# Optimization experiments

Measured on AMD Instinct MI355X. Metric: run time of the kernel, lower is better.

Reference implementation:

```python
import jax, jax.numpy as jnp
import numpy as np

N_NODES = 25000
N_EDGES = 400000
IN = 128
HID = [64, 64, 128]
HEADS = [4, 4, 1]
SLOPE = 0.01  # F.leaky_relu default


def _xavier(key, shape):
    fan_out, fan_in = shape
    std = (2.0 / (fan_in + fan_out)) ** 0.5
    return std * jax.random.normal(key, shape, dtype=jnp.float32)


def setup_inputs() -> dict:
    key = jax.random.key(0)
    ks = jax.random.split(key, 24)
    inp = {}
    inp['x'] = jax.random.normal(ks[0], (N_NODES, IN), dtype=jnp.float32)
    inp['edge_weight'] = jax.random.uniform(ks[1], (N_EDGES,), dtype=jnp.float32)
    inp['edge_src'] = jax.random.randint(ks[2], (N_EDGES,), 0, N_NODES)
    inp['edge_dst'] = jax.random.randint(ks[3], (N_EDGES,), 0, N_NODES)
    inp['pos_src'] = jax.random.randint(ks[4], (100000,), 0, N_NODES)
    inp['pos_dst'] = jax.random.randint(ks[5], (100000,), 0, N_NODES)
    inp['neg_src'] = jax.random.randint(ks[6], (100000,), 0, N_NODES)
    inp['neg_dst'] = jax.random.randint(ks[7], (100000,), 0, N_NODES)
    # GAT layer params: fc weight [H*F, in], attn vector [F], bias [H*F]
    dims_in = [IN, HID[0] * HEADS[0], HID[1] * HEADS[1]]
    for l in range(3):
        H, F = HEADS[l], HID[l]
        inp[f'W{l}'] = _xavier(ks[8 + 2 * l], (H * F, dims_in[l]))
        inp[f'a{l}'] = _xavier(ks[9 + 2 * l], (1, F)).reshape(F)
        inp[f'b{l}'] = jnp.zeros((H * F,), dtype=jnp.float32)
    # predictor MLP: 128 -> 64 -> 32 -> 1 (Linear with bias)
    d = HID[2]
    inp['pW1'] = _xavier(ks[14], (d // 2, d)); inp['pb1'] = jnp.zeros((d // 2,), jnp.float32)
    inp['pW2'] = _xavier(ks[15], (d // 4, d // 2)); inp['pb2'] = jnp.zeros((d // 4,), jnp.float32)
    inp['pW3'] = _xavier(ks[16], (1, d // 4)); inp['pb3'] = jnp.zeros((1,), jnp.float32)
    return inp


def _leaky(x, slope=SLOPE):
    return jnp.where(x >= 0, x, slope * x)


def _gat_layer(x, W, a, b, src, dst, ew, H, F):
    N = x.shape[0]
    h = (x @ W.T).reshape(N, H, F)               # [N,H,F]
    hs = h[src]                                   # [E,H,F] gathered src feats
    # GATv2-style score: attn_fc(q_src + k_dst) per head
    score = jnp.einsum('ehf,f->eh', hs + h[dst], a)   # [E,H]
    e = _leaky(score + jnp.log1p(ew)[:, None])         # [E,H]
    # segment softmax over edges grouped by destination node
    m = jax.ops.segment_max(e, dst, num_segments=N)    # [N,H]
    m = jnp.where(jnp.isfinite(m), m, 0.0)             # guard empty segments
    ex = jnp.exp(e - m[dst])
    s = jax.ops.segment_sum(ex, dst, num_segments=N)   # [N,H]
    alpha = ex / jnp.maximum(s[dst], 1e-20)            # [E,H]
    out = jax.ops.segment_sum(alpha[:, :, None] * hs, dst, num_segments=N)  # [N,H,F]
    return out.reshape(N, H * F) + b


def _predictor(z, pW1, pb1, pW2, pb2, pW3, pb3):
    z = _leaky(z @ pW1.T + pb1, 0.2)
    z = _leaky(z @ pW2.T + pb2, 0.2)
    return z @ pW3.T + pb3


def reference(x, edge_weight, W0, a0, b0, W1, a1, b1, W2, a2, b2,
              pW1, pb1, pW2, pb2, pW3, pb3,
              edge_src, edge_dst, pos_src, pos_dst, neg_src, neg_dst):
    h = _gat_layer(x, W0, a0, b0, edge_src, edge_dst, edge_weight, HEADS[0], HID[0])
    h = _leaky(h)
    h = _gat_layer(h, W1, a1, b1, edge_src, edge_dst, edge_weight, HEADS[1], HID[1])
    h = _leaky(h)
    h = _gat_layer(h, W2, a2, b2, edge_src, edge_dst, edge_weight, HEADS[2], HID[2])
    gat_embedding = h
    h_pos = _predictor(h[pos_src] * h[pos_dst], pW1, pb1, pW2, pb2, pW3, pb3)
    h_neg = _predictor(h[neg_src] * h[neg_dst], pW1, pb1, pW2, pb2, pW3, pb3)
    return (h_pos, h_neg, gat_embedding)
```

## Files before the change

kernel.cpp:

```cpp
#include <hip/hip_runtime.h>
#include <math.h>

#define N_IN 128

__device__ __forceinline__ float leaky01(float x) { return x >= 0.f ? x : 0.01f * x; }
__device__ __forceinline__ float leaky02(float x) { return x >= 0.f ? x : 0.2f * x; }

__global__ void k_count(const int* __restrict__ edst, int* __restrict__ deg, int E) {
    int e = blockIdx.x * 256 + threadIdx.x;
    if (e < E) atomicAdd(&deg[edst[e]], 1);
}

__global__ void k_scan1(const int* __restrict__ deg, int* __restrict__ rowptr,
                        int* __restrict__ bsum, int n) {
    __shared__ int s[256];
    int b = blockIdx.x, t = threadIdx.x;
    int idx = b * 256 + t;
    int v = (idx < n) ? deg[idx] : 0;
    s[t] = v;
    __syncthreads();
    for (int off = 1; off < 256; off <<= 1) {
        int x = (t >= off) ? s[t - off] : 0;
        __syncthreads();
        s[t] += x;
        __syncthreads();
    }
    if (idx < n) rowptr[idx + 1] = s[t];
    if (t == 255) bsum[b] = s[255];
}

__global__ void k_scan2(const int* __restrict__ bsum, int* __restrict__ boff, int nb) {
    __shared__ int s[128];
    int t = threadIdx.x;
    int v = (t < nb) ? bsum[t] : 0;
    s[t] = v;
    __syncthreads();
    for (int off = 1; off < 128; off <<= 1) {
        int x = (t >= off) ? s[t - off] : 0;
        __syncthreads();
        s[t] += x;
        __syncthreads();
    }
    if (t < nb) boff[t] = s[t] - v;
}

__global__ void k_scan3(int* __restrict__ rowptr, const int* __restrict__ boff, int n) {
    int idx = blockIdx.x * 256 + threadIdx.x;
    if (idx < n) rowptr[idx + 1] += boff[idx >> 8];
    if (idx == 0) rowptr[0] = 0;
}

__global__ void k_fill(const int* __restrict__ esrc, const int* __restrict__ edst,
                       const float* __restrict__ ew, const int* __restrict__ rowptr,
                       int* __restrict__ cursor, int* __restrict__ eid,
                       int* __restrict__ csrc, float* __restrict__ clew, int E) {
    int e = blockIdx.x * 256 + threadIdx.x;
    if (e >= E) return;
    int d = edst[e];
    int slot = rowptr[d] + atomicAdd(&cursor[d], 1);
    eid[slot] = e;
    csrc[slot] = esrc[e];
    clew[slot] = log1pf(ew[e]);
}

__global__ void k_sortseg(const int* __restrict__ rowptr, int* __restrict__ eid,
                          int* __restrict__ csrc, float* __restrict__ clew, int n) {
    int v = blockIdx.x * 256 + threadIdx.x;
    if (v >= n) return;
    int b = rowptr[v], e = rowptr[v + 1];
    for (int i = b + 1; i < e; i++) {
        int ke = eid[i], ks = csrc[i];
        float kl = clew[i];
        int j = i - 1;
        while (j >= b && eid[j] > ke) {
            eid[j + 1] = eid[j]; csrc[j + 1] = csrc[j]; clew[j + 1] = clew[j];
            j--;
        }
        eid[j + 1] = ke; csrc[j + 1] = ks; clew[j + 1] = kl;
    }
}

__global__ __launch_bounds__(256) void k_gemm(const float* __restrict__ X,
                                              const float* __restrict__ W,
                                              float* __restrict__ C,
                                              int N, int K, int M,
                                              const float* __restrict__ avec,
                                              float* __restrict__ qaOut,
                                              int H, int F) {
    __shared__ float Xs[16][68];
    __shared__ float Ws[16][132];
    __shared__ float qred[64][17];
    int r0 = blockIdx.y * 64;
    int c0 = blockIdx.x * 128;
    int t = threadIdx.x;
    int ty = t >> 4, tx = t & 15;

    float acc[4][8];
#pragma unroll
    for (int i = 0; i < 4; i++)
#pragma unroll
        for (int j = 0; j < 8; j++) acc[i][j] = 0.f;

    int lr = t >> 2;
    int lk = (t & 3) * 4;
    bool xok = (r0 + lr) < N;
    const float* Xp = X + (size_t)(r0 + lr) * K + lk;
    int wr = t >> 1;
    int wk = (t & 1) * 8;
    const float* Wp = W + (size_t)(c0 + wr) * K + wk;

    for (int k0 = 0; k0 < K; k0 += 16) {
        float4 xv = xok ? *(const float4*)(Xp + k0) : make_float4(0.f, 0.f, 0.f, 0.f);
        float4 wv0 = *(const float4*)(Wp + k0);
        float4 wv1 = *(const float4*)(Wp + k0 + 4);
        __syncthreads();
        Xs[lk + 0][lr] = xv.x; Xs[lk + 1][lr] = xv.y;
        Xs[lk + 2][lr] = xv.z; Xs[lk + 3][lr] = xv.w;
        Ws[wk + 0][wr] = wv0.x; Ws[wk + 1][wr] = wv0.y;
        Ws[wk + 2][wr] = wv0.z; Ws[wk + 3][wr] = wv0.w;
        Ws[wk + 4][wr] = wv1.x; Ws[wk + 5][wr] = wv1.y;
        Ws[wk + 6][wr] = wv1.z; Ws[wk + 7][wr] = wv1.w;
        __syncthreads();
#pragma unroll
        for (int k = 0; k < 16; k++) {
            float4 a = *(const float4*)&Xs[k][ty * 4];
            float4 b0 = *(const float4*)&Ws[k][tx * 8];
            float4 b1 = *(const float4*)&Ws[k][tx * 8 + 4];
            float av[4] = {a.x, a.y, a.z, a.w};
            float bv[8] = {b0.x, b0.y, b0.z, b0.w, b1.x, b1.y, b1.z, b1.w};
#pragma unroll
            for (int i = 0; i < 4; i++)
#pragma unroll
                for (int j = 0; j < 8; j++) acc[i][j] += av[i] * bv[j];
        }
    }

#pragma unroll
    for (int i = 0; i < 4; i++) {
        int row = r0 + ty * 4 + i;
        if (row < N) {
            float4 v0 = make_float4(acc[i][0], acc[i][1], acc[i][2], acc[i][3]);
            float4 v1 = make_float4(acc[i][4], acc[i][5], acc[i][6], acc[i][7]);
            *(float4*)&C[(size_t)row * M + c0 + tx * 8] = v0;
            *(float4*)&C[(size_t)row * M + c0 + tx * 8 + 4] = v1;
        }
    }

    if (qaOut) {
        int f0 = (c0 + tx * 8) & (F - 1);
        float4 a0 = *(const float4*)&avec[f0];
        float4 a1 = *(const float4*)&avec[f0 + 4];
#pragma unroll
        for (int i = 0; i < 4; i++) {
            float s = acc[i][0] * a0.x + acc[i][1] * a0.y + acc[i][2] * a0.z + acc[i][3] * a0.w
                    + acc[i][4] * a1.x + acc[i][5] * a1.y + acc[i][6] * a1.z + acc[i][7] * a1.w;
            qred[ty * 4 + i][tx] = s;
        }
        __syncthreads();
        if (t < 64) {
            int R = r0 + t;
            if (R < N) {
                float s0 = 0.f, s1 = 0.f;
#pragma unroll
                for (int x = 0; x < 8; x++) { s0 += qred[t][x]; s1 += qred[t][x + 8]; }
                if (F == 64) {
                    int hb = c0 >> 6;
                    qaOut[(size_t)R * H + hb] = s0;
                    qaOut[(size_t)R * H + hb + 1] = s1;
                } else {
                    qaOut[R] = s0 + s1;
                }
            }
        }
    }
}

template <int H, int F, int VW, bool LOUT>
__global__ __launch_bounds__(256) void k_fagg(const float* __restrict__ feat,
                                              const float* __restrict__ qa,
                                              const float* __restrict__ bias,
                                              const int* __restrict__ rowptr,
                                              const int* __restrict__ csr_src,
                                              const float* __restrict__ csr_lew,
                                              float* __restrict__ out, int N) {
    constexpr int M = H * F;
    constexpr int CACHE = 128;
    constexpr int EPP = 64 / H;
    __shared__ int sh_src[4][CACHE];
    __shared__ float sh_sc[4][CACHE * H];
    int w = threadIdx.x >> 6, l = threadIdx.x & 63;
    int n = blockIdx.x * 4 + w;
    if (n >= N) return;
    int beg = rowptr[n];
    int deg = rowptr[n + 1] - beg;
    int c = l * VW;
    const int hh = c / F;

    float acc0[VW], acc1[VW];
#pragma unroll
    for (int j = 0; j < VW; j++) { acc0[j] = 0.f; acc1[j] = 0.f; }

    if (deg > 0) {
        if (deg <= CACHE) {
            const int e0 = l / H;
            const int h = l & (H - 1);
            float qd = qa[(size_t)n * H + h];
            float mx = -1e30f;
            for (int i0 = 0; i0 < deg; i0 += EPP) {
                int e = i0 + e0;
                if (e < deg) {
                    int src = csr_src[beg + e];
                    float lw = csr_lew[beg + e];
                    if (h == 0) sh_src[w][e] = src;
                    float sc = leaky01(qa[(size_t)src * H + h] + qd + lw);
                    sh_sc[w][e * H + h] = sc;
                    mx = fmaxf(mx, sc);
                }
            }
            for (int off = 32; off >= H; off >>= 1)
                mx = fmaxf(mx, __shfl_xor(mx, off, 64));
            float sm = 0.f;
            for (int i0 = 0; i0 < deg; i0 += EPP) {
                int e = i0 + e0;
                if (e < deg) sm += __expf(sh_sc[w][e * H + h] - mx);
            }
            for (int off = 32; off >= H; off >>= 1)
                sm += __shfl_xor(sm, off, 64);
            float inv = 1.f / fmaxf(sm, 1e-20f);
            for (int i0 = 0; i0 < deg; i0 += EPP) {
                int e = i0 + e0;
                if (e < deg)
                    sh_sc[w][e * H + h] = __expf(sh_sc[w][e * H + h] - mx) * inv;
            }
            int i = 0;
            for (; i + 4 <= deg; i += 4) {
                int s0 = sh_src[w][i], s1 = sh_src[w][i + 1];
                int s2 = sh_src[w][i + 2], s3 = sh_src[w][i + 3];
                float a0 = sh_sc[w][i * H + hh], a1 = sh_sc[w][(i + 1) * H + hh];
                float a2 = sh_sc[w][(i + 2) * H + hh], a3 = sh_sc[w][(i + 3) * H + hh];
                float f0[VW], f1[VW], f2[VW], f3[VW];
                if (VW == 4) {
                    float4 v0 = *(const float4*)&feat[(size_t)s0 * M + c];
                    float4 v1 = *(const float4*)&feat[(size_t)s1 * M + c];
                    float4 v2 = *(const float4*)&feat[(size_t)s2 * M + c];
                    float4 v3 = *(const float4*)&feat[(size_t)s3 * M + c];
                    f0[0] = v0.x; f0[1] = v0.y; f0[2] = v0.z; f0[3] = v0.w;
                    f1[0] = v1.x; f1[1] = v1.y; f1[2] = v1.z; f1[3] = v1.w;
                    f2[0] = v2.x; f2[1] = v2.y; f2[2] = v2.z; f2[3] = v2.w;
                    f3[0] = v3.x; f3[1] = v3.y; f3[2] = v3.z; f3[3] = v3.w;
                } else {
                    float2 v0 = *(const float2*)&feat[(size_t)s0 * M + c];
                    float2 v1 = *(const float2*)&feat[(size_t)s1 * M + c];
                    float2 v2 = *(const float2*)&feat[(size_t)s2 * M + c];
                    float2 v3 = *(const float2*)&feat[(size_t)s3 * M + c];
                    f0[0] = v0.x; f0[1] = v0.y;
                    f1[0] = v1.x; f1[1] = v1.y;
                    f2[0] = v2.x; f2[1] = v2.y;
                    f3[0] = v3.x; f3[1] = v3.y;
                }
#pragma unroll
                for (int j = 0; j < VW; j++) {
                    acc0[j] += a0 * f0[j] + a1 * f1[j];
                    acc1[j] += a2 * f2[j] + a3 * f3[j];
                }
            }
            for (; i < deg; ++i) {
                int s0 = sh_src[w][i];
                float a0 = sh_sc[w][i * H + hh];
                if (VW == 4) {
                    float4 v0 = *(const float4*)&feat[(size_t)s0 * M + c];
                    acc0[0] += a0 * v0.x; acc0[1] += a0 * v0.y;
                    acc0[2] += a0 * v0.z; acc0[3] += a0 * v0.w;
                } else {
                    float2 v0 = *(const float2*)&feat[(size_t)s0 * M + c];
                    acc0[0] += a0 * v0.x; acc0[1] += a0 * v0.y;
                }
            }
        } else {
            float qd[H];
#pragma unroll
            for (int h = 0; h < H; h++) qd[h] = qa[(size_t)n * H + h];
            int end = beg + deg;
            float mx[H];
#pragma unroll
            for (int h = 0; h < H; h++) mx[h] = -1e30f;
            for (int i = beg + l; i < end; i += 64) {
                int src = csr_src[i];
                float lw = csr_lew[i];
#pragma unroll
                for (int h = 0; h < H; h++)
                    mx[h] = fmaxf(mx[h], leaky01(qa[(size_t)src * H + h] + qd[h] + lw));
            }
#pragma unroll
            for (int h = 0; h < H; h++) {
                for (int off = 32; off > 0; off >>= 1)
                    mx[h] = fmaxf(mx[h], __shfl_xor(mx[h], off, 64));
            }
            float sm[H];
#pragma unroll
            for (int h = 0; h < H; h++) sm[h] = 0.f;
            for (int i = beg + l; i < end; i += 64) {
                int src = csr_src[i];
                float lw = csr_lew[i];
#pragma unroll
                for (int h = 0; h < H; h++)
                    sm[h] += __expf(leaky01(qa[(size_t)src * H + h] + qd[h] + lw) - mx[h]);
            }
#pragma unroll
            for (int h = 0; h < H; h++) {
                for (int off = 32; off > 0; off >>= 1)
                    sm[h] += __shfl_xor(sm[h], off, 64);
            }
            float inv[H];
#pragma unroll
            for (int h = 0; h < H; h++) inv[h] = 1.f / fmaxf(sm[h], 1e-20f);

            for (int c0 = 0; c0 < deg; c0 += 64) {
                int cn = min(64, deg - c0);
                if (l < cn) {
                    int src = csr_src[beg + c0 + l];
                    float lw = csr_lew[beg + c0 + l];
                    sh_src[w][l] = src;
#pragma unroll
                    for (int h = 0; h < H; h++)
                        sh_sc[w][l * H + h] =
                            __expf(leaky01(qa[(size_t)src * H + h] + qd[h] + lw) - mx[h]) * inv[h];
                }
                for (int i = 0; i < cn; i++) {
                    int s0 = sh_src[w][i];
                    float a0 = sh_sc[w][i * H + hh];
                    if (VW == 4) {
                        float4 v0 = *(const float4*)&feat[(size_t)s0 * M + c];
                        acc0[0] += a0 * v0.x; acc0[1] += a0 * v0.y;
                        acc0[2] += a0 * v0.z; acc0[3] += a0 * v0.w;
                    } else {
                        float2 v0 = *(const float2*)&feat[(size_t)s0 * M + c];
                        acc0[0] += a0 * v0.x; acc0[1] += a0 * v0.y;
                    }
                }
            }
        }
    }

#pragma unroll
    for (int j = 0; j < VW; j++) {
        float r = acc0[j] + acc1[j] + bias[c + j];
        if (LOUT) r = leaky01(r);
        out[(size_t)n * M + c + j] = r;
    }
}

__global__ __launch_bounds__(256) void k_predf6(const float* __restrict__ h2,
                                                const int* __restrict__ ps, const int* __restrict__ pd,
                                                const int* __restrict__ ns, const int* __restrict__ nd,
                                                const float* __restrict__ W1, const float* __restrict__ b1,
                                                const float* __restrict__ W2, const float* __restrict__ b2,
                                                const float* __restrict__ W3, const float* __restrict__ b3,
                                                float* __restrict__ out, int npos, int ntot) {
    __shared__ float Zs[128 * 36];
    __shared__ float Wc[32 * 68];
    __shared__ int sp[128], dp[128];

    int t = threadIdx.x;
    int p0 = blockIdx.x * 128;
    int ty2 = t >> 3;
    int tx2 = t & 7;

    if (t < 128) {
        int pr = p0 + t;
        int s = 0, d = 0;
        if (pr < ntot) {
            if (pr < npos) { s = ps[pr]; d = pd[pr]; }
            else           { s = ns[pr - npos]; d = nd[pr - npos]; }
        }
        sp[t] = s; dp[t] = d;
    }
    __syncthreads();

    float acc[4][8];
#pragma unroll
    for (int i = 0; i < 4; i++)
#pragma unroll
        for (int j = 0; j < 8; j++) acc[i][j] = 0.f;

    int sr = t >> 3;
    int sq = t & 7;

    for (int kc = 0; kc < 128; kc += 32) {
#pragma unroll
        for (int it = 0; it < 4; ++it) {
            int r = it * 32 + sr;
            int s = sp[r], d = dp[r];
            float4 a = *(const float4*)&h2[(size_t)s * 128 + kc + sq * 4];
            float4 b = *(const float4*)&h2[(size_t)d * 128 + kc + sq * 4];
            *(float4*)&Zs[r * 36 + sq * 4] =
                make_float4(a.x * b.x, a.y * b.y, a.z * b.z, a.w * b.w);
        }
        {
            int out_ = t & 63;
            int kh = (t >> 6) * 8;
            const float* wr = W1 + (size_t)out_ * 128 + kc + kh;
#pragma unroll
            for (int c = 0; c < 2; c++) {
                float4 wv = *(const float4*)(wr + c * 4);
                Wc[(kh + c * 4 + 0) * 68 + out_] = wv.x;
                Wc[(kh + c * 4 + 1) * 68 + out_] = wv.y;
                Wc[(kh + c * 4 + 2) * 68 + out_] = wv.z;
                Wc[(kh + c * 4 + 3) * 68 + out_] = wv.w;
            }
        }
        __syncthreads();
#pragma unroll
        for (int k4 = 0; k4 < 8; ++k4) {
            float4 a4[4];
#pragma unroll
            for (int i = 0; i < 4; i++)
                a4[i] = *(const float4*)&Zs[(ty2 + 32 * i) * 36 + k4 * 4];
#pragma unroll
            for (int kk = 0; kk < 4; ++kk) {
                float4 bA = *(const float4*)&Wc[(k4 * 4 + kk) * 68 + tx2 * 8];
                float4 bB = *(const float4*)&Wc[(k4 * 4 + kk) * 68 + tx2 * 8 + 4];
                float bv[8] = {bA.x, bA.y, bA.z, bA.w, bB.x, bB.y, bB.z, bB.w};
#pragma unroll
                for (int i = 0; i < 4; i++) {
                    float a = (kk == 0) ? a4[i].x : (kk == 1) ? a4[i].y : (kk == 2) ? a4[i].z : a4[i].w;
#pragma unroll
                    for (int j = 0; j < 8; j++) acc[i][j] += a * bv[j];
                }
            }
        }
        __syncthreads();
    }

    {
        float4 b1a = *(const float4*)&b1[tx2 * 8];
        float4 b1b = *(const float4*)&b1[tx2 * 8 + 4];
        float bb[8] = {b1a.x, b1a.y, b1a.z, b1a.w, b1b.x, b1b.y, b1b.z, b1b.w};
#pragma unroll
        for (int i = 0; i < 4; i++)
#pragma unroll
            for (int j = 0; j < 8; j++) acc[i][j] += bb[j];
    }

    float t2[32];
#pragma unroll
    for (int o = 0; o < 32; o++) t2[o] = b2[o];

    if (tx2 < 4) {
#pragma unroll
        for (int i = 0; i < 4; i++) {
            int row = ty2 + 32 * i;
            *(float4*)&Zs[row * 36 + tx2 * 8] =
                make_float4(acc[i][0], acc[i][1], acc[i][2], acc[i][3]);
            *(float4*)&Zs[row * 36 + tx2 * 8 + 4] =
                make_float4(acc[i][4], acc[i][5], acc[i][6], acc[i][7]);
        }
    }
    __syncthreads();
    if (t < 128) {
        for (int j = 0; j < 32; j += 4) {
            float4 v4 = *(const float4*)&Zs[t * 36 + j];
            float v0 = leaky02(v4.x), v1 = leaky02(v4.y), v2 = leaky02(v4.z), v3 = leaky02(v4.w);
#pragma unroll
            for (int o = 0; o < 32; o++) {
                const float* w2 = W2 + (size_t)o * 64 + j;
                t2[o] += v0 * w2[0] + v1 * w2[1] + v2 * w2[2] + v3 * w2[3];
            }
        }
    }
    __syncthreads();
    if (tx2 >= 4) {
#pragma unroll
        for (int i = 0; i < 4; i++) {
            int row = ty2 + 32 * i;
            *(float4*)&Zs[row * 36 + (tx2 - 4) * 8] =
                make_float4(acc[i][0], acc[i][1], acc[i][2], acc[i][3]);
            *(float4*)&Zs[row * 36 + (tx2 - 4) * 8 + 4] =
                make_float4(acc[i][4], acc[i][5], acc[i][6], acc[i][7]);
        }
    }
    __syncthreads();
    if (t < 128) {
        for (int j = 0; j < 32; j += 4) {
            float4 v4 = *(const float4*)&Zs[t * 36 + j];
            float v0 = leaky02(v4.x), v1 = leaky02(v4.y), v2 = leaky02(v4.z), v3 = leaky02(v4.w);
#pragma unroll
            for (int o = 0; o < 32; o++) {
                const float* w2 = W2 + (size_t)o * 64 + 32 + j;
                t2[o] += v0 * w2[0] + v1 * w2[1] + v2 * w2[2] + v3 * w2[3];
            }
        }
        float o3 = b3[0];
#pragma unroll
        for (int o = 0; o < 32; o++) o3 += leaky02(t2[o]) * W3[o];
        if (p0 + t < ntot) out[p0 + t] = o3;
    }
}

extern "C" void kernel_launch(void* const* d_in, const int* in_sizes, int n_in,
                              void* d_out, int out_size, void* d_ws, size_t ws_size,
                              hipStream_t stream) {
    const float* x    = (const float*)d_in[0];
    const float* ew   = (const float*)d_in[1];
    const int* esrc   = (const int*)d_in[2];
    const int* edst   = (const int*)d_in[3];
    const int* pos_s  = (const int*)d_in[4];
    const int* pos_d  = (const int*)d_in[5];
    const int* neg_s  = (const int*)d_in[6];
    const int* neg_d  = (const int*)d_in[7];
    const float* W0 = (const float*)d_in[8];
    const float* a0 = (const float*)d_in[9];
    const float* b0 = (const float*)d_in[10];
    const float* W1 = (const float*)d_in[11];
    const float* a1 = (const float*)d_in[12];
    const float* b1 = (const float*)d_in[13];
    const float* W2 = (const float*)d_in[14];
    const float* a2 = (const float*)d_in[15];
    const float* b2 = (const float*)d_in[16];
    const float* pW1 = (const float*)d_in[17];
    const float* pb1 = (const float*)d_in[18];
    const float* pW2 = (const float*)d_in[19];
    const float* pb2 = (const float*)d_in[20];
    const float* pW3 = (const float*)d_in[21];
    const float* pb3 = (const float*)d_in[22];

    const int N = in_sizes[0] / N_IN;
    const int E = in_sizes[1];
    const int NP = in_sizes[4];

    size_t off = 0;
    auto alloc = [&](size_t bytes) {
        void* p = (char*)d_ws + off;
        off += (bytes + 255) & ~(size_t)255;
        return p;
    };
    int* deg      = (int*)alloc((size_t)N * 4);
    int* cursor   = (int*)alloc((size_t)N * 4);
    int* rowptr   = (int*)alloc((size_t)(N + 1) * 4);
    int* bsum     = (int*)alloc(512);
    int* boff     = (int*)alloc(512);
    int* csr_eid  = (int*)alloc((size_t)E * 4);
    int* csr_src  = (int*)alloc((size_t)E * 4);
    float* csr_lew = (float*)alloc((size_t)E * 4);
    float* qa     = (float*)alloc((size_t)N * 4 * 4);
    float* A      = (float*)alloc((size_t)N * 256 * 4);
    float* B      = (float*)alloc((size_t)N * 256 * 4);
    (void)ws_size; (void)n_in; (void)out_size;

    float* out_pred = (float*)d_out;
    float* emb      = (float*)d_out + 2 * NP;

    hipMemsetAsync(deg, 0, (size_t)N * 4, stream);
    hipMemsetAsync(cursor, 0, (size_t)N * 4, stream);

    int eb = (E + 255) / 256;
    int nb = (N + 255) / 256;
    k_count<<<eb, 256, 0, stream>>>(edst, deg, E);
    k_scan1<<<nb, 256, 0, stream>>>(deg, rowptr, bsum, N);
    k_scan2<<<1, 128, 0, stream>>>(bsum, boff, nb);
    k_scan3<<<nb, 256, 0, stream>>>(rowptr, boff, N);
    k_fill<<<eb, 256, 0, stream>>>(esrc, edst, ew, rowptr, cursor, csr_eid, csr_src, csr_lew, E);
    k_sortseg<<<(N + 255) / 256, 256, 0, stream>>>(rowptr, csr_eid, csr_src, csr_lew, N);

    int rb = (N + 63) / 64;
    int sb = (N + 3) / 4;

    k_gemm<<<dim3(2, rb), 256, 0, stream>>>(x, W0, A, N, 128, 256, a0, qa, 4, 64);
    k_fagg<4, 64, 4, true><<<sb, 256, 0, stream>>>(A, qa, b0, rowptr, csr_src, csr_lew, B, N);

    k_gemm<<<dim3(2, rb), 256, 0, stream>>>(B, W1, A, N, 256, 256, a1, qa, 4, 64);
    k_fagg<4, 64, 4, true><<<sb, 256, 0, stream>>>(A, qa, b1, rowptr, csr_src, csr_lew, B, N);

    k_gemm<<<dim3(1, rb), 256, 0, stream>>>(B, W2, A, N, 256, 128, a2, qa, 1, 128);
    k_fagg<1, 128, 2, false><<<sb, 256, 0, stream>>>(A, qa, b2, rowptr, csr_src, csr_lew, emb, N);

    int ntot = 2 * NP;
    k_predf6<<<(ntot + 127) / 128, 256, 0, stream>>>(emb, pos_s, pos_d, neg_s, neg_d,
                                                     pW1, pb1, pW2, pb2, pW3, pb3,
                                                     out_pred, NP, ntot);
}
```

Before: 487.8 us.

## Pack CSR into int4 records, warp-parallel segment sort, smaller predictor tiles

Edge id, source and log1p weight are packed into one int4 CSR record, so k_fill does one store per edge and the aggregation kernels do one 16-byte load instead of separate arrays. The per-node serial insertion sort runs one thread per node; it is replaced by a wavefront-per-node rank sort using shuffles for degree up to 64, with a single-lane fallback for larger segments. The predictor kernel tile shrinks from 128 to 64 pairs per block to launch more blocks. The packing adds 4 unused bytes per edge, raising CSR bandwidth in the aggregation kernels.

```diff
diff --git a/kernel.cpp b/kernel.cpp
--- a/kernel.cpp
+++ b/kernel.cpp
@@ -1,5 +1,6 @@
 #include <hip/hip_runtime.h>
 #include <math.h>
+#include <limits.h>
 
 #define N_IN 128
 
@@ -52,31 +53,41 @@
 
 __global__ void k_fill(const int* __restrict__ esrc, const int* __restrict__ edst,
                        const float* __restrict__ ew, const int* __restrict__ rowptr,
-                       int* __restrict__ cursor, int* __restrict__ eid,
-                       int* __restrict__ csrc, float* __restrict__ clew, int E) {
+                       int* __restrict__ cursor, int4* __restrict__ csr, int E) {
     int e = blockIdx.x * 256 + threadIdx.x;
     if (e >= E) return;
     int d = edst[e];
     int slot = rowptr[d] + atomicAdd(&cursor[d], 1);
-    eid[slot] = e;
-    csrc[slot] = esrc[e];
-    clew[slot] = log1pf(ew[e]);
-}
-
-__global__ void k_sortseg(const int* __restrict__ rowptr, int* __restrict__ eid,
-                          int* __restrict__ csrc, float* __restrict__ clew, int n) {
-    int v = blockIdx.x * 256 + threadIdx.x;
+    csr[slot] = make_int4(e, esrc[e], __float_as_int(log1pf(ew[e])), 0);
+}
+
+__global__ __launch_bounds__(256) void k_sortw(const int* __restrict__ rowptr,
+                                               int4* __restrict__ csr, int n) {
+    int w = threadIdx.x >> 6, l = threadIdx.x & 63;
+    int v = blockIdx.x * 4 + w;
     if (v >= n) return;
     int b = rowptr[v], e = rowptr[v + 1];
-    for (int i = b + 1; i < e; i++) {
-        int ke = eid[i], ks = csrc[i];
-        float kl = clew[i];
-        int j = i - 1;
-        while (j >= b && eid[j] > ke) {
-            eid[j + 1] = eid[j]; csrc[j + 1] = csrc[j]; clew[j + 1] = clew[j];
-            j--;
-        }
-        eid[j + 1] = ke; csrc[j + 1] = ks; clew[j + 1] = kl;
+    int deg = e - b;
+    if (deg <= 1) return;
+    if (deg <= 64) {
+        int4 rec = make_int4(INT_MAX, 0, 0, 0);
+        if (l < deg) rec = csr[b + l];
+        int rank = 0;
+        for (int j = 0; j < 64; j++) {
+            int ej = __shfl(rec.x, j, 64);
+            rank += (ej < rec.x) ? 1 : 0;
+        }
+        if (l < deg) csr[b + rank] = rec;
+    } else if (l == 0) {
+        for (int i = b + 1; i < e; i++) {
+            int4 k = csr[i];
+            int j = i - 1;
+            while (j >= b && csr[j].x > k.x) {
+                csr[j + 1] = csr[j];
+                j--;
+            }
+            csr[j + 1] = k;
+        }
     }
 }
 
@@ -180,8 +191,7 @@
                                               const float* __restrict__ qa,
                                               const float* __restrict__ bias,
                                               const int* __restrict__ rowptr,
-                                              const int* __restrict__ csr_src,
-                                              const float* __restrict__ csr_lew,
+                                              const int4* __restrict__ csr,
                                               float* __restrict__ out, int N) {
     constexpr int M = H * F;
     constexpr int CACHE = 128;
@@ -209,10 +219,10 @@
             for (int i0 = 0; i0 < deg; i0 += EPP) {
                 int e = i0 + e0;
                 if (e < deg) {
-                    int src = csr_src[beg + e];
-                    float lw = csr_lew[beg + e];
-                    if (h == 0) sh_src[w][e] = src;
-                    float sc = leaky01(qa[(size_t)src * H + h] + qd + lw);
+                    int4 q = csr[beg + e];
+                    float lw = __int_as_float(q.z);
+                    if (h == 0) sh_src[w][e] = q.y;
+                    float sc = leaky01(qa[(size_t)q.y * H + h] + qd + lw);
                     sh_sc[w][e * H + h] = sc;
                     mx = fmaxf(mx, sc);
                 }
@@ -285,11 +295,11 @@
 #pragma unroll
             for (int h = 0; h < H; h++) mx[h] = -1e30f;
             for (int i = beg + l; i < end; i += 64) {
-                int src = csr_src[i];
-                float lw = csr_lew[i];
+                int4 q = csr[i];
+                float lw = __int_as_float(q.z);
 #pragma unroll
                 for (int h = 0; h < H; h++)
-                    mx[h] = fmaxf(mx[h], leaky01(qa[(size_t)src * H + h] + qd[h] + lw));
+                    mx[h] = fmaxf(mx[h], leaky01(qa[(size_t)q.y * H + h] + qd[h] + lw));
             }
 #pragma unroll
             for (int h = 0; h < H; h++) {
@@ -300,11 +310,11 @@
 #pragma unroll
             for (int h = 0; h < H; h++) sm[h] = 0.f;
             for (int i = beg + l; i < end; i += 64) {
-                int src = csr_src[i];
-                float lw = csr_lew[i];
+                int4 q = csr[i];
+                float lw = __int_as_float(q.z);
 #pragma unroll
                 for (int h = 0; h < H; h++)
-                    sm[h] += __expf(leaky01(qa[(size_t)src * H + h] + qd[h] + lw) - mx[h]);
+                    sm[h] += __expf(leaky01(qa[(size_t)q.y * H + h] + qd[h] + lw) - mx[h]);
             }
 #pragma unroll
             for (int h = 0; h < H; h++) {
@@ -318,13 +328,13 @@
             for (int c0 = 0; c0 < deg; c0 += 64) {
                 int cn = min(64, deg - c0);
                 if (l < cn) {
-                    int src = csr_src[beg + c0 + l];
-                    float lw = csr_lew[beg + c0 + l];
-                    sh_src[w][l] = src;
+                    int4 q = csr[beg + c0 + l];
+                    float lw = __int_as_float(q.z);
+                    sh_src[w][l] = q.y;
 #pragma unroll
                     for (int h = 0; h < H; h++)
                         sh_sc[w][l * H + h] =
-                            __expf(leaky01(qa[(size_t)src * H + h] + qd[h] + lw) - mx[h]) * inv[h];
+                            __expf(leaky01(qa[(size_t)q.y * H + h] + qd[h] + lw) - mx[h]) * inv[h];
                 }
                 for (int i = 0; i < cn; i++) {
                     int s0 = sh_src[w][i];
@@ -350,23 +360,23 @@
     }
 }
 
-__global__ __launch_bounds__(256) void k_predf6(const float* __restrict__ h2,
+__global__ __launch_bounds__(256) void k_predf7(const float* __restrict__ h2,
                                                 const int* __restrict__ ps, const int* __restrict__ pd,
                                                 const int* __restrict__ ns, const int* __restrict__ nd,
                                                 const float* __restrict__ W1, const float* __restrict__ b1,
                                                 const float* __restrict__ W2, const float* __restrict__ b2,
                                                 const float* __restrict__ W3, const float* __restrict__ b3,
                                                 float* __restrict__ out, int npos, int ntot) {
-    __shared__ float Zs[128 * 36];
+    __shared__ float Zs[64 * 36];
     __shared__ float Wc[32 * 68];
-    __shared__ int sp[128], dp[128];
+    __shared__ int sp[64], dp[64];
 
     int t = threadIdx.x;
-    int p0 = blockIdx.x * 128;
+    int p0 = blockIdx.x * 64;
     int ty2 = t >> 3;
     int tx2 = t & 7;
 
-    if (t < 128) {
+    if (t < 64) {
         int pr = p0 + t;
         int s = 0, d = 0;
         if (pr < ntot) {
@@ -377,9 +387,9 @@
     }
     __syncthreads();
 
-    float acc[4][8];
-#pragma unroll
-    for (int i = 0; i < 4; i++)
+    float acc[2][8];
+#pragma unroll
+    for (int i = 0; i < 2; i++)
 #pragma unroll
         for (int j = 0; j < 8; j++) acc[i][j] = 0.f;
 
@@ -388,7 +398,7 @@
 
     for (int kc = 0; kc < 128; kc += 32) {
 #pragma unroll
-        for (int it = 0; it < 4; ++it) {
+        for (int it = 0; it < 2; ++it) {
             int r = it * 32 + sr;
             int s = sp[r], d = dp[r];
             float4 a = *(const float4*)&h2[(size_t)s * 128 + kc + sq * 4];
@@ -412,9 +422,9 @@
         __syncthreads();
 #pragma unroll
         for (int k4 = 0; k4 < 8; ++k4) {
-            float4 a4[4];
-#pragma unroll
-            for (int i = 0; i < 4; i++)
+            float4 a4[2];
+#pragma unroll
+            for (int i = 0; i < 2; i++)
                 a4[i] = *(const float4*)&Zs[(ty2 + 32 * i) * 36 + k4 * 4];
 #pragma unroll
             for (int kk = 0; kk < 4; ++kk) {
@@ -422,7 +432,7 @@
                 float4 bB = *(const float4*)&Wc[(k4 * 4 + kk) * 68 + tx2 * 8 + 4];
                 float bv[8] = {bA.x, bA.y, bA.z, bA.w, bB.x, bB.y, bB.z, bB.w};
 #pragma unroll
-                for (int i = 0; i < 4; i++) {
+                for (int i = 0; i < 2; i++) {
                     float a = (kk == 0) ? a4[i].x : (kk == 1) ? a4[i].y : (kk == 2) ? a4[i].z : a4[i].w;
 #pragma unroll
                     for (int j = 0; j < 8; j++) acc[i][j] += a * bv[j];
@@ -437,7 +447,7 @@
         float4 b1b = *(const float4*)&b1[tx2 * 8 + 4];
         float bb[8] = {b1a.x, b1a.y, b1a.z, b1a.w, b1b.x, b1b.y, b1b.z, b1b.w};
 #pragma unroll
-        for (int i = 0; i < 4; i++)
+        for (int i = 0; i < 2; i++)
 #pragma unroll
             for (int j = 0; j < 8; j++) acc[i][j] += bb[j];
     }
@@ -448,7 +458,7 @@
 
     if (tx2 < 4) {
 #pragma unroll
-        for (int i = 0; i < 4; i++) {
+        for (int i = 0; i < 2; i++) {
             int row = ty2 + 32 * i;
             *(float4*)&Zs[row * 36 + tx2 * 8] =
                 make_float4(acc[i][0], acc[i][1], acc[i][2], acc[i][3]);
@@ -457,7 +467,7 @@
         }
     }
     __syncthreads();
-    if (t < 128) {
+    if (t < 64) {
         for (int j = 0; j < 32; j += 4) {
             float4 v4 = *(const float4*)&Zs[t * 36 + j];
             float v0 = leaky02(v4.x), v1 = leaky02(v4.y), v2 = leaky02(v4.z), v3 = leaky02(v4.w);
@@ -471,7 +481,7 @@
     __syncthreads();
     if (tx2 >= 4) {
 #pragma unroll
-        for (int i = 0; i < 4; i++) {
+        for (int i = 0; i < 2; i++) {
             int row = ty2 + 32 * i;
             *(float4*)&Zs[row * 36 + (tx2 - 4) * 8] =
                 make_float4(acc[i][0], acc[i][1], acc[i][2], acc[i][3]);
@@ -480,7 +490,7 @@
         }
     }
     __syncthreads();
-    if (t < 128) {
+    if (t < 64) {
         for (int j = 0; j < 32; j += 4) {
             float4 v4 = *(const float4*)&Zs[t * 36 + j];
             float v0 = leaky02(v4.x), v1 = leaky02(v4.y), v2 = leaky02(v4.z), v3 = leaky02(v4.w);
@@ -539,9 +549,7 @@
     int* rowptr   = (int*)alloc((size_t)(N + 1) * 4);
     int* bsum     = (int*)alloc(512);
     int* boff     = (int*)alloc(512);
-    int* csr_eid  = (int*)alloc((size_t)E * 4);
-    int* csr_src  = (int*)alloc((size_t)E * 4);
-    float* csr_lew = (float*)alloc((size_t)E * 4);
+    int4* csr     = (int4*)alloc((size_t)E * 16);
     float* qa     = (float*)alloc((size_t)N * 4 * 4);
     float* A      = (float*)alloc((size_t)N * 256 * 4);
     float* B      = (float*)alloc((size_t)N * 256 * 4);
@@ -559,23 +567,23 @@
     k_scan1<<<nb, 256, 0, stream>>>(deg, rowptr, bsum, N);
     k_scan2<<<1, 128, 0, stream>>>(bsum, boff, nb);
     k_scan3<<<nb, 256, 0, stream>>>(rowptr, boff, N);
-    k_fill<<<eb, 256, 0, stream>>>(esrc, edst, ew, rowptr, cursor, csr_eid, csr_src, csr_lew, E);
-    k_sortseg<<<(N + 255) / 256, 256, 0, stream>>>(rowptr, csr_eid, csr_src, csr_lew, N);
+    k_fill<<<eb, 256, 0, stream>>>(esrc, edst, ew, rowptr, cursor, csr, E);
+    k_sortw<<<(N + 3) / 4, 256, 0, stream>>>(rowptr, csr, N);
 
     int rb = (N + 63) / 64;
     int sb = (N + 3) / 4;
 
     k_gemm<<<dim3(2, rb), 256, 0, stream>>>(x, W0, A, N, 128, 256, a0, qa, 4, 64);
-    k_fagg<4, 64, 4, true><<<sb, 256, 0, stream>>>(A, qa, b0, rowptr, csr_src, csr_lew, B, N);
+    k_fagg<4, 64, 4, true><<<sb, 256, 0, stream>>>(A, qa, b0, rowptr, csr, B, N);
 
     k_gemm<<<dim3(2, rb), 256, 0, stream>>>(B, W1, A, N, 256, 256, a1, qa, 4, 64);
-    k_fagg<4, 64, 4, true><<<sb, 256, 0, stream>>>(A, qa, b1, rowptr, csr_src, csr_lew, B, N);
+    k_fagg<4, 64, 4, true><<<sb, 256, 0, stream>>>(A, qa, b1, rowptr, csr, B, N);
 
     k_gemm<<<dim3(1, rb), 256, 0, stream>>>(B, W2, A, N, 256, 128, a2, qa, 1, 128);
-    k_fagg<1, 128, 2, false><<<sb, 256, 0, stream>>>(A, qa, b2, rowptr, csr_src, csr_lew, emb, N);
+    k_fagg<1, 128, 2, false><<<sb, 256, 0, stream>>>(A, qa, b2, rowptr, csr, emb, N);
 
     int ntot = 2 * NP;
-    k_predf6<<<(ntot + 127) / 128, 256, 0, stream>>>(emb, pos_s, pos_d, neg_s, neg_d,
-                                                     pW1, pb1, pW2, pb2, pW3, pb3,
-                                                     out_pred, NP, ntot);
-}
+    k_predf7<<<(ntot + 63) / 64, 256, 0, stream>>>(emb, pos_s, pos_d, neg_s, neg_d,
+                                                   pW1, pb1, pW2, pb2, pW3, pb3,
+                                                   out_pred, NP, ntot);
+}
```

Result: faster. 427.4 us (-12.4%).
